# Kernel tuning notes

Hardware: AMD Instinct MI355X
Metric: run time of the kernel (lower is better)

Reference implementation:

```python
import jax, jax.numpy as jnp
import numpy as np

# Static problem structure (matches setup_inputs)
B, NPOLY, VPP, L = 32, 256, 64, 32
LAYERS = 3
PLEN = L * 2 ** LAYERS  # 256
LN_EPS = 1e-5


def _layernorm(h, g, b):
    mu = h.mean(-1, keepdims=True)
    var = ((h - mu) ** 2).mean(-1, keepdims=True)
    return g * (h - mu) / jnp.sqrt(var + LN_EPS) + b


def _forward(data, W0, b0, g0, beta0, W1, b1, g1, beta1, W2, b2, g2, beta2,
             Wq, bq, Wk, bk, Wv, bv):
    # row 0 holds agent polyline index in feature 0
    agent_id = data[:, 0, 0].astype(jnp.int32)  # [B]
    vecs = data[:, 1:, :]
    vecs = vecs.at[:, :, -1].set(0.0)  # zero out polyline-id feature (data[:,:,-1]=0)
    x = vecs.reshape(B, NPOLY, VPP, L)  # uniform polyline groups

    # SubGraph: 3 layers of (MLP -> maxpool aggregate -> concat), doubling width
    for (W, b, g, be) in ((W0, b0, g0, beta0), (W1, b1, g1, beta1), (W2, b2, g2, beta2)):
        h = jax.nn.relu(_layernorm(x @ W + b, g, be))  # [B,P,V,c]
        agg = h.max(axis=2, keepdims=True)             # [B,P,1,c]
        x = jnp.concatenate([h, jnp.broadcast_to(agg, h.shape)], axis=-1)  # [B,P,V,2c]
    P = x.max(axis=2)  # [B, NPOLY, PLEN] polyline features

    # Global graph: single-head attention with agent polyline as query
    q = P[jnp.arange(B), agent_id] @ Wq + bq          # [B, C]
    k = P @ Wk + bk                                    # [B, P, C]
    v = P @ Wv + bv
    scores = jnp.einsum('bc,bpc->bp', q, k) / jnp.sqrt(jnp.float32(PLEN))
    att = jax.nn.softmax(scores, axis=-1)
    return jnp.einsum('bp,bpc->bc', att, v)           # [B, PLEN]


def setup_inputs() -> dict:
    key = jax.random.key(0)
    ks = jax.random.split(key, 24)
    V = 1 + NPOLY * VPP
    data = jax.random.normal(ks[0], (B, V, L), dtype=jnp.float32)
    agent = jax.random.randint(ks[1], (B,), 0, NPOLY).astype(jnp.float32)
    data = data.at[:, 0, :].set(0.0).at[:, 0, 0].set(agent)
    pid = jnp.repeat(jnp.arange(NPOLY), VPP).astype(jnp.float32)
    data = data.at[:, 1:, -1].set(pid[None, :])

    inp = {'data': data}
    c = L
    for i in range(LAYERS):
        inp[f'W{i}'] = 0.02 * jax.random.normal(ks[2 + i], (c, c), dtype=jnp.float32)
        inp[f'b{i}'] = jnp.zeros((c,), jnp.float32)
        inp[f'g{i}'] = jnp.ones((c,), jnp.float32)
        inp[f'beta{i}'] = jnp.zeros((c,), jnp.float32)
        c *= 2
    C = PLEN
    for j, nm in enumerate(('q', 'k', 'v')):
        inp[f'W{nm}'] = 0.02 * jax.random.normal(ks[10 + j], (C, C), dtype=jnp.float32)
        inp[f'b{nm}'] = jnp.zeros((C,), jnp.float32)
    return inp


def reference(data, W0, b0, g0, beta0, W1, b1, g1, beta1, W2, b2, g2, beta2,
              Wq, bq, Wk, bk, Wv, bv):
    return _forward(data, W0, b0, g0, beta0, W1, b1, g1, beta1, W2, b2, g2, beta2,
                    Wq, bq, Wk, bk, Wv, bv)
```

## Files before the change

### kernel.cpp

```cpp
#include <hip/hip_runtime.h>

#define NPOLY 256
#define VPP   64
#define LCH   32
#define NV    (1 + NPOLY * VPP)
#define LN_EPS 1e-5f

typedef __bf16 bf16x8 __attribute__((ext_vector_type(8)));
typedef float  f32x4  __attribute__((ext_vector_type(4)));

union U4B8 { uint4 u; bf16x8 v; };

__device__ __forceinline__ unsigned packbf(float a, float b) {
    unsigned r;
    asm("v_cvt_pk_bf16_f32 %0, %1, %2" : "=v"(r) : "v"(a), "v"(b));
    return r;
}

__global__ void vn_prep1(const float* __restrict__ W0, const float* __restrict__ W1,
                         const float* __restrict__ W2,
                         const float* __restrict__ Wq, const float* __restrict__ Wk,
                         const float* __restrict__ Wv,
                         float* __restrict__ Wqf, float* __restrict__ Wkf,
                         float* __restrict__ Wvf, uint4* __restrict__ wpack)
{
    int t = blockIdx.x * 256 + threadIdx.x;
    if (t < 3 * 32768) {
        int which = t >> 15, r = t & 32767;
        const float* src = which == 0 ? Wq : which == 1 ? Wk : Wv;
        float*       dst = which == 0 ? Wqf : which == 1 ? Wkf : Wvf;
        dst[r] = src[r] + src[r + 128 * 256];
        return;
    }
    t -= 3 * 32768;
    if (t >= 22 * 64) return;
    int f = t >> 6, L = t & 63, q = L >> 4, m = L & 15;
    const float* src; int N, k0, col;
    if (f < 2)      { src = W0; N = 32;  k0 = q * 8;                 col = f * 16 + m; }
    else if (f < 6) { src = W1; N = 64;  k0 = q * 8;                 col = (f - 2) * 16 + m; }
    else { int g = f - 6; src = W2; N = 128; k0 = (g >> 3) * 32 + q * 8; col = (g & 7) * 16 + m; }
    float e[8];
    #pragma unroll
    for (int j = 0; j < 8; j++) e[j] = src[(k0 + j) * N + col];
    uint4 o;
    o.x = packbf(e[0], e[1]); o.y = packbf(e[2], e[3]);
    o.z = packbf(e[4], e[5]); o.w = packbf(e[6], e[7]);
    wpack[f * 64 + L] = o;
}

__global__ void vn_prep2(const float* __restrict__ Wqf, const float* __restrict__ Wkf,
                         const float* __restrict__ bq,
                         float* __restrict__ Mff, float* __restrict__ u0f)
{
    int t = blockIdx.x * 256 + threadIdx.x;
    if (t < 16384) {
        int i = t >> 7, j = t & 127;
        const float4* a = (const float4*)(Wqf + i * 256);
        const float4* b = (const float4*)(Wkf + j * 256);
        float s0 = 0.f, s1 = 0.f, s2 = 0.f, s3 = 0.f;
        #pragma unroll 4
        for (int c = 0; c < 64; c++) {
            float4 A = a[c], B = b[c];
            s0 = fmaf(A.x, B.x, s0); s1 = fmaf(A.y, B.y, s1);
            s2 = fmaf(A.z, B.z, s2); s3 = fmaf(A.w, B.w, s3);
        }
        Mff[i * 128 + j] = (s0 + s1) + (s2 + s3);
    } else if (t < 16512) {
        int j = t - 16384;
        const float4* a = (const float4*)bq;
        const float4* b = (const float4*)(Wkf + j * 256);
        float s0 = 0.f, s1 = 0.f, s2 = 0.f, s3 = 0.f;
        #pragma unroll 4
        for (int c = 0; c < 64; c++) {
            float4 A = a[c], B = b[c];
            s0 = fmaf(A.x, B.x, s0); s1 = fmaf(A.y, B.y, s1);
            s2 = fmaf(A.z, B.z, s2); s3 = fmaf(A.w, B.w, s3);
        }
        u0f[j] = (s0 + s1) + (s2 + s3);
    }
}

__global__ __launch_bounds__(64, 3) void vn_mlp(
    const float* __restrict__ data, const uint4* __restrict__ wpack,
    const float* __restrict__ b0, const float* __restrict__ g0, const float* __restrict__ be0,
    const float* __restrict__ W1, const float* __restrict__ b1,
    const float* __restrict__ g1, const float* __restrict__ be1,
    const float* __restrict__ W2, const float* __restrict__ b2,
    const float* __restrict__ g2, const float* __restrict__ be2,
    float* __restrict__ Ph)
{
    __shared__ __align__(16) unsigned short hbuf[64 * 72];
    __shared__ float fbuf[192];

    const int blk = blockIdx.x;
    const int L = threadIdx.x, q = L >> 4, m = L & 15;
    const int bb = blk >> 8, pp = blk & 255;

    const float* rowbase = data + ((size_t)bb * NV + 1 + (size_t)pp * VPP) * LCH;
    bf16x8 A0[4];
    #pragma unroll
    for (int rt = 0; rt < 4; rt++) {
        const float* rp = rowbase + (size_t)(rt * 16 + m) * LCH + q * 8;
        float4 u = *(const float4*)rp;
        float4 v = *(const float4*)(rp + 4);
        if (q == 3) v.w = 0.f;
        U4B8 c;
        c.u.x = packbf(u.x, u.y); c.u.y = packbf(u.z, u.w);
        c.u.z = packbf(v.x, v.y); c.u.w = packbf(v.z, v.w);
        A0[rt] = c.v;
    }
    U4B8 t0, t1; t0.u = wpack[0 * 64 + L]; t1.u = wpack[1 * 64 + L];
    float bc0[2] = { b0[m], b0[16 + m] };
    f32x4 acc0[4][2];
    #pragma unroll
    for (int rt = 0; rt < 4; rt++) {
        {
            f32x4 a = { bc0[0], bc0[0], bc0[0], bc0[0] };
            acc0[rt][0] = __builtin_amdgcn_mfma_f32_16x16x32_bf16(A0[rt], t0.v, a, 0, 0, 0);
        }
        {
            f32x4 a = { bc0[1], bc0[1], bc0[1], bc0[1] };
            acc0[rt][1] = __builtin_amdgcn_mfma_f32_16x16x32_bf16(A0[rt], t1.v, a, 0, 0, 0);
        }
    }
    float g0c[2]  = { g0[m],  g0[16 + m]  };
    float be0c[2] = { be0[m], be0[16 + m] };
    float a0mx[2] = { 0.f, 0.f };
    #pragma unroll
    for (int rt = 0; rt < 4; rt++) {
        #pragma unroll
        for (int reg = 0; reg < 4; reg++) {
            float x0 = acc0[rt][0][reg], x1 = acc0[rt][1][reg];
            float rs = x0 + x1, rq = x0 * x0 + x1 * x1;
            #pragma unroll
            for (int s = 1; s < 16; s <<= 1) { rs += __shfl_xor(rs, s, 64); rq += __shfl_xor(rq, s, 64); }
            float mu = rs * (1.f / 32.f);
            float var = rq * (1.f / 32.f) - mu * mu;
            float ri = rsqrtf(var + LN_EPS);
            #pragma unroll
            for (int ct = 0; ct < 2; ct++) {
                float v = fmaxf(fmaf(g0c[ct] * ri, acc0[rt][ct][reg] - mu, be0c[ct]), 0.f);
                acc0[rt][ct][reg] = v;
                a0mx[ct] = fmaxf(a0mx[ct], v);
            }
        }
    }
    #pragma unroll
    for (int ct = 0; ct < 2; ct++) {
        float v = a0mx[ct];
        v = fmaxf(v, __shfl_xor(v, 16, 64));
        v = fmaxf(v, __shfl_xor(v, 32, 64));
        a0mx[ct] = v;
    }
    if (q == 0) { fbuf[m] = a0mx[0]; fbuf[16 + m] = a0mx[1]; }
    __builtin_amdgcn_wave_barrier();
    float au1a = b1[L], au1b = 0.f;
    for (int j = 0; j < 32; j += 2) {
        au1a = fmaf(fbuf[j],     W1[(32 + j) * 64 + L],     au1a);
        au1b = fmaf(fbuf[j + 1], W1[(32 + j + 1) * 64 + L], au1b);
    }
    float au1 = au1a + au1b;
    #pragma unroll
    for (int rt = 0; rt < 4; rt++)
        #pragma unroll
        for (int reg = 0; reg < 4; reg++) {
            int row = rt * 16 + q * 4 + reg;
            unsigned u = packbf(acc0[rt][0][reg], acc0[rt][1][reg]);
            hbuf[row * 72 + m]      = (unsigned short)u;
            hbuf[row * 72 + 16 + m] = (unsigned short)(u >> 16);
        }
    __builtin_amdgcn_wave_barrier();
    fbuf[64 + L] = au1;
    __builtin_amdgcn_wave_barrier();

    bf16x8 A1[4];
    #pragma unroll
    for (int rt = 0; rt < 4; rt++) {
        U4B8 c; c.u = *(const uint4*)(hbuf + (rt * 16 + m) * 72 + q * 8);
        A1[rt] = c.v;
    }
    f32x4 acc1[4][4];
    #pragma unroll
    for (int ct = 0; ct < 4; ct++) {
        U4B8 wv; wv.u = wpack[(2 + ct) * 64 + L];
        float au = fbuf[64 + ct * 16 + m];
        #pragma unroll
        for (int rt = 0; rt < 4; rt++) {
            f32x4 a = { au, au, au, au };
            acc1[rt][ct] = __builtin_amdgcn_mfma_f32_16x16x32_bf16(A1[rt], wv.v, a, 0, 0, 0);
        }
    }
    float g1c[4], be1c[4];
    #pragma unroll
    for (int ct = 0; ct < 4; ct++) { g1c[ct] = g1[ct * 16 + m]; be1c[ct] = be1[ct * 16 + m]; }
    float a1mx[4] = { 0.f, 0.f, 0.f, 0.f };
    #pragma unroll
    for (int rt = 0; rt < 4; rt++) {
        #pragma unroll
        for (int reg = 0; reg < 4; reg++) {
            float rs = 0.f, rq = 0.f;
            #pragma unroll
            for (int ct = 0; ct < 4; ct++) { float x = acc1[rt][ct][reg]; rs += x; rq += x * x; }
            #pragma unroll
            for (int s = 1; s < 16; s <<= 1) { rs += __shfl_xor(rs, s, 64); rq += __shfl_xor(rq, s, 64); }
            float mu = rs * (1.f / 64.f);
            float var = rq * (1.f / 64.f) - mu * mu;
            float ri = rsqrtf(var + LN_EPS);
            #pragma unroll
            for (int ct = 0; ct < 4; ct++) {
                float v = fmaxf(fmaf(g1c[ct] * ri, acc1[rt][ct][reg] - mu, be1c[ct]), 0.f);
                acc1[rt][ct][reg] = v;
                a1mx[ct] = fmaxf(a1mx[ct], v);
            }
        }
    }
    #pragma unroll
    for (int ct = 0; ct < 4; ct++) {
        float v = a1mx[ct];
        v = fmaxf(v, __shfl_xor(v, 16, 64));
        v = fmaxf(v, __shfl_xor(v, 32, 64));
        a1mx[ct] = v;
    }
    __builtin_amdgcn_wave_barrier();
    if (q == 0) {
        #pragma unroll
        for (int ct = 0; ct < 4; ct++) fbuf[ct * 16 + m] = a1mx[ct];
    }
    __builtin_amdgcn_wave_barrier();
    float au2a = b2[L], au2b = b2[64 + L], au2c = 0.f, au2d = 0.f;
    for (int j = 0; j < 64; j += 2) {
        float av0 = fbuf[j], av1 = fbuf[j + 1];
        au2a = fmaf(av0, W2[(64 + j) * 128 + L],          au2a);
        au2b = fmaf(av0, W2[(64 + j) * 128 + 64 + L],     au2b);
        au2c = fmaf(av1, W2[(64 + j + 1) * 128 + L],      au2c);
        au2d = fmaf(av1, W2[(64 + j + 1) * 128 + 64 + L], au2d);
    }
    au2a += au2c; au2b += au2d;
    #pragma unroll
    for (int rt = 0; rt < 4; rt++)
        #pragma unroll
        for (int reg = 0; reg < 4; reg++) {
            int row = rt * 16 + q * 4 + reg;
            unsigned ua = packbf(acc1[rt][0][reg], acc1[rt][1][reg]);
            unsigned ub = packbf(acc1[rt][2][reg], acc1[rt][3][reg]);
            hbuf[row * 72 + m]      = (unsigned short)ua;
            hbuf[row * 72 + 16 + m] = (unsigned short)(ua >> 16);
            hbuf[row * 72 + 32 + m] = (unsigned short)ub;
            hbuf[row * 72 + 48 + m] = (unsigned short)(ub >> 16);
        }
    __builtin_amdgcn_wave_barrier();
    fbuf[64 + L] = au2a; fbuf[128 + L] = au2b;
    __builtin_amdgcn_wave_barrier();

    bf16x8 A2[4][2];
    #pragma unroll
    for (int rt = 0; rt < 4; rt++)
        #pragma unroll
        for (int ks = 0; ks < 2; ks++) {
            U4B8 c; c.u = *(const uint4*)(hbuf + (rt * 16 + m) * 72 + ks * 32 + q * 8);
            A2[rt][ks] = c.v;
        }
    f32x4 rsum[4] = {}, rqsum[4] = {};
    #pragma unroll
    for (int ct = 0; ct < 8; ct++) {
        U4B8 wa, wb;
        wa.u = wpack[(6 + ct) * 64 + L];
        wb.u = wpack[(14 + ct) * 64 + L];
        float au = fbuf[64 + ct * 16 + m];
        #pragma unroll
        for (int rt = 0; rt < 4; rt++) {
            f32x4 a = { au, au, au, au };
            a = __builtin_amdgcn_mfma_f32_16x16x32_bf16(A2[rt][0], wa.v, a, 0, 0, 0);
            a = __builtin_amdgcn_mfma_f32_16x16x32_bf16(A2[rt][1], wb.v, a, 0, 0, 0);
            rsum[rt] += a;
            rqsum[rt] += a * a;
        }
    }
    f32x4 muv[4], riv[4];
    #pragma unroll
    for (int rt = 0; rt < 4; rt++) {
        #pragma unroll
        for (int reg = 0; reg < 4; reg++) {
            float rs = rsum[rt][reg], rq = rqsum[rt][reg];
            #pragma unroll
            for (int s = 1; s < 16; s <<= 1) { rs += __shfl_xor(rs, s, 64); rq += __shfl_xor(rq, s, 64); }
            float mu = rs * (1.f / 128.f);
            float var = rq * (1.f / 128.f) - mu * mu;
            muv[rt][reg] = mu;
            riv[rt][reg] = rsqrtf(var + LN_EPS);
        }
    }
    float g2c[8], be2c[8];
    #pragma unroll
    for (int ct = 0; ct < 8; ct++) { g2c[ct] = g2[ct * 16 + m]; be2c[ct] = be2[ct * 16 + m]; }
    float m2[8] = { 0.f, 0.f, 0.f, 0.f, 0.f, 0.f, 0.f, 0.f };
    #pragma unroll
    for (int ct = 0; ct < 8; ct++) {
        U4B8 wa, wb;
        wa.u = wpack[(6 + ct) * 64 + L];
        wb.u = wpack[(14 + ct) * 64 + L];
        float au = fbuf[64 + ct * 16 + m];
        #pragma unroll
        for (int rt = 0; rt < 4; rt++) {
            f32x4 a = { au, au, au, au };
            a = __builtin_amdgcn_mfma_f32_16x16x32_bf16(A2[rt][0], wa.v, a, 0, 0, 0);
            a = __builtin_amdgcn_mfma_f32_16x16x32_bf16(A2[rt][1], wb.v, a, 0, 0, 0);
            #pragma unroll
            for (int reg = 0; reg < 4; reg++) {
                float v = fmaxf(fmaf(g2c[ct] * riv[rt][reg], a[reg] - muv[rt][reg], be2c[ct]), 0.f);
                m2[ct] = fmaxf(m2[ct], v);
            }
        }
    }
    #pragma unroll
    for (int ct = 0; ct < 8; ct++) {
        float v = m2[ct];
        v = fmaxf(v, __shfl_xor(v, 16, 64));
        v = fmaxf(v, __shfl_xor(v, 32, 64));
        m2[ct] = v;
    }
    float v1 = q == 0 ? m2[0] : q == 1 ? m2[1] : q == 2 ? m2[2] : m2[3];
    float v2 = q == 0 ? m2[4] : q == 1 ? m2[5] : q == 2 ? m2[6] : m2[7];
    float* op = Ph + (size_t)blk * 128;
    op[L] = v1; op[64 + L] = v2;
}

__global__ __launch_bounds__(256) void vn_attn(
    const float* __restrict__ data, const float* __restrict__ Ph,
    const float* __restrict__ Mff, const float* __restrict__ u0f,
    const float* __restrict__ Wvf, const float* __restrict__ bv,
    float* __restrict__ out)
{
    __shared__ __align__(16) float pah[128], tts[128], att[256], pb[128];
    __shared__ __align__(16) float part[256];
    __shared__ float red[8];
    const int b = blockIdx.x, tid = threadIdx.x, lane = tid & 63, wave = tid >> 6;
    const float* PhB = Ph + (size_t)b * NPOLY * 128;
    const int agent = (int)data[(size_t)b * NV * LCH];

    if (tid < 128) pah[tid] = PhB[(size_t)agent * 128 + tid];
    __syncthreads();

    {
        const int j = tid & 127, h = tid >> 7;
        const float* mc = Mff + (size_t)(h * 64) * 128 + j;
        const float* pv = pah + h * 64;
        float s0 = 0.f, s1 = 0.f, s2 = 0.f, s3 = 0.f;
        for (int i = 0; i < 64; i += 4) {
            s0 = fmaf(pv[i],     mc[(i)     * 128], s0);
            s1 = fmaf(pv[i + 1], mc[(i + 1) * 128], s1);
            s2 = fmaf(pv[i + 2], mc[(i + 2) * 128], s2);
            s3 = fmaf(pv[i + 3], mc[(i + 3) * 128], s3);
        }
        part[tid] = (s0 + s1) + (s2 + s3);
    }
    __syncthreads();
    if (tid < 128) tts[tid] = part[tid] + part[128 + tid] + u0f[tid];
    __syncthreads();

    float sv;
    {
        const float* pr = PhB + (size_t)tid * 128;
        float s0 = 0.f, s1 = 0.f, s2 = 0.f, s3 = 0.f;
        for (int j = 0; j < 128; j += 16) {
            float4 x0 = *(const float4*)(pr + j);
            float4 x1 = *(const float4*)(pr + j + 4);
            float4 x2 = *(const float4*)(pr + j + 8);
            float4 x3 = *(const float4*)(pr + j + 12);
            float4 t0 = *(const float4*)(tts + j);
            float4 t1 = *(const float4*)(tts + j + 4);
            float4 t2 = *(const float4*)(tts + j + 8);
            float4 t3 = *(const float4*)(tts + j + 12);
            s0 = fmaf(x0.w, t0.w, fmaf(x0.z, t0.z, fmaf(x0.y, t0.y, fmaf(x0.x, t0.x, s0))));
            s1 = fmaf(x1.w, t1.w, fmaf(x1.z, t1.z, fmaf(x1.y, t1.y, fmaf(x1.x, t1.x, s1))));
            s2 = fmaf(x2.w, t2.w, fmaf(x2.z, t2.z, fmaf(x2.y, t2.y, fmaf(x2.x, t2.x, s2))));
            s3 = fmaf(x3.w, t3.w, fmaf(x3.z, t3.z, fmaf(x3.y, t3.y, fmaf(x3.x, t3.x, s3))));
        }
        sv = ((s0 + s1) + (s2 + s3)) * 0.0625f;
    }
    float mx = sv;
    #pragma unroll
    for (int s = 1; s < 64; s <<= 1) mx = fmaxf(mx, __shfl_xor(mx, s, 64));
    if (lane == 0) red[wave] = mx;
    __syncthreads();
    mx = fmaxf(fmaxf(red[0], red[1]), fmaxf(red[2], red[3]));
    float e = expf(sv - mx);
    float sm = e;
    #pragma unroll
    for (int s = 1; s < 64; s <<= 1) sm += __shfl_xor(sm, s, 64);
    if (lane == 0) red[4 + wave] = sm;
    __syncthreads();
    const float tot = red[4] + red[5] + red[6] + red[7];
    att[tid] = e / tot;
    __syncthreads();

    {
        const int c = tid & 127, h = tid >> 7;
        const float* pp = PhB + (size_t)(h * 128) * 128 + c;
        const float* ap = att + h * 128;
        float s0 = 0.f, s1 = 0.f, s2 = 0.f, s3 = 0.f;
        for (int p = 0; p < 128; p += 4) {
            s0 = fmaf(ap[p],     pp[(p)     * 128], s0);
            s1 = fmaf(ap[p + 1], pp[(p + 1) * 128], s1);
            s2 = fmaf(ap[p + 2], pp[(p + 2) * 128], s2);
            s3 = fmaf(ap[p + 3], pp[(p + 3) * 128], s3);
        }
        part[tid] = (s0 + s1) + (s2 + s3);
    }
    __syncthreads();
    if (tid < 128) pb[tid] = part[tid] + part[128 + tid];
    __syncthreads();

    {
        const float* wv = Wvf + tid;
        float s0 = 0.f, s1 = 0.f, s2 = 0.f, s3 = 0.f;
        for (int j = 0; j < 128; j += 4) {
            s0 = fmaf(pb[j],     wv[(j)     * 256], s0);
            s1 = fmaf(pb[j + 1], wv[(j + 1) * 256], s1);
            s2 = fmaf(pb[j + 2], wv[(j + 2) * 256], s2);
            s3 = fmaf(pb[j + 3], wv[(j + 3) * 256], s3);
        }
        out[(size_t)b * 256 + tid] = bv[tid] + ((s0 + s1) + (s2 + s3));
    }
}

extern "C" void kernel_launch(void* const* d_in, const int* in_sizes, int n_in,
                              void* d_out, int out_size, void* d_ws, size_t ws_size,
                              hipStream_t stream)
{
    const float* data = (const float*)d_in[0];
    const float* W0 = (const float*)d_in[1];
    const float* b0 = (const float*)d_in[2];
    const float* g0 = (const float*)d_in[3];
    const float* be0= (const float*)d_in[4];
    const float* W1 = (const float*)d_in[5];
    const float* b1 = (const float*)d_in[6];
    const float* g1 = (const float*)d_in[7];
    const float* be1= (const float*)d_in[8];
    const float* W2 = (const float*)d_in[9];
    const float* b2 = (const float*)d_in[10];
    const float* g2 = (const float*)d_in[11];
    const float* be2= (const float*)d_in[12];
    const float* Wq = (const float*)d_in[13];
    const float* bq = (const float*)d_in[14];
    const float* Wk = (const float*)d_in[15];
    const float* bk = (const float*)d_in[16];
    const float* Wv = (const float*)d_in[17];
    const float* bv = (const float*)d_in[18];
    (void)bk;

    char* wsb = (char*)d_ws;
    float* Ph    = (float*)(wsb);
    float* Wqf   = (float*)(wsb + 4194304);
    float* Wkf   = (float*)(wsb + 4325376);
    float* Wvf   = (float*)(wsb + 4456448);
    float* Mff   = (float*)(wsb + 4587520);
    float* u0f   = (float*)(wsb + 4653056);
    uint4* wpack = (uint4*)(wsb + 4653568);

    vn_prep1<<<390, 256, 0, stream>>>(W0, W1, W2, Wq, Wk, Wv, Wqf, Wkf, Wvf, wpack);
    vn_prep2<<<65, 256, 0, stream>>>(Wqf, Wkf, bq, Mff, u0f);
    vn_mlp<<<32 * NPOLY, 64, 0, stream>>>(data, wpack,
                                          b0, g0, be0,
                                          W1, b1, g1, be1,
                                          W2, b2, g2, be2, Ph);
    vn_attn<<<32, 256, 0, stream>>>(data, Ph, Mff, u0f, Wvf, bv, (float*)d_out);
}
```

Baseline: 234.1 us.

## Split per-polyline MLP across four waves with shared-memory max and matvec reductions

Each polyline block moves from a single 64-thread wave that handled all four 16-row tiles to four waves of 256 threads, one row tile each. The cross-row max-pool and the aggregate matvec through W1 and W2 are now split across the waves through shared partial buffers and block-level barriers. Because each wave now holds all layer-2 accumulators in registers, the second MFMA pass used for layernorm in layer 2 is dropped. The aim is more parallelism and fewer registers per wave, at the price of several __syncthreads per block and more shared memory.

Result: faster. 209.8 us (-10.4%).

```diff
diff --git a/kernel.cpp b/kernel.cpp
--- a/kernel.cpp
+++ b/kernel.cpp
@@ -80,7 +80,7 @@
     }
 }
 
-__global__ __launch_bounds__(64, 3) void vn_mlp(
+__global__ __launch_bounds__(256, 3) void vn_mlp(
     const float* __restrict__ data, const uint4* __restrict__ wpack,
     const float* __restrict__ b0, const float* __restrict__ g0, const float* __restrict__ be0,
     const float* __restrict__ W1, const float* __restrict__ b1,
@@ -90,47 +90,43 @@
     float* __restrict__ Ph)
 {
     __shared__ __align__(16) unsigned short hbuf[64 * 72];
-    __shared__ float fbuf[192];
-
+    __shared__ float partA[4][128];
+    __shared__ float partB[4][128];
+
+    const int tid = threadIdx.x;
+    const int w = tid >> 6, L = tid & 63, q = L >> 4, m = L & 15;
     const int blk = blockIdx.x;
-    const int L = threadIdx.x, q = L >> 4, m = L & 15;
     const int bb = blk >> 8, pp = blk & 255;
+    const int r0 = w * 16;
 
     const float* rowbase = data + ((size_t)bb * NV + 1 + (size_t)pp * VPP) * LCH;
-    bf16x8 A0[4];
-    #pragma unroll
-    for (int rt = 0; rt < 4; rt++) {
-        const float* rp = rowbase + (size_t)(rt * 16 + m) * LCH + q * 8;
+    bf16x8 A0;
+    {
+        const float* rp = rowbase + (size_t)(r0 + m) * LCH + q * 8;
         float4 u = *(const float4*)rp;
         float4 v = *(const float4*)(rp + 4);
         if (q == 3) v.w = 0.f;
         U4B8 c;
         c.u.x = packbf(u.x, u.y); c.u.y = packbf(u.z, u.w);
         c.u.z = packbf(v.x, v.y); c.u.w = packbf(v.z, v.w);
-        A0[rt] = c.v;
-    }
-    U4B8 t0, t1; t0.u = wpack[0 * 64 + L]; t1.u = wpack[1 * 64 + L];
-    float bc0[2] = { b0[m], b0[16 + m] };
-    f32x4 acc0[4][2];
-    #pragma unroll
-    for (int rt = 0; rt < 4; rt++) {
-        {
-            f32x4 a = { bc0[0], bc0[0], bc0[0], bc0[0] };
-            acc0[rt][0] = __builtin_amdgcn_mfma_f32_16x16x32_bf16(A0[rt], t0.v, a, 0, 0, 0);
-        }
-        {
-            f32x4 a = { bc0[1], bc0[1], bc0[1], bc0[1] };
-            acc0[rt][1] = __builtin_amdgcn_mfma_f32_16x16x32_bf16(A0[rt], t1.v, a, 0, 0, 0);
-        }
-    }
-    float g0c[2]  = { g0[m],  g0[16 + m]  };
-    float be0c[2] = { be0[m], be0[16 + m] };
-    float a0mx[2] = { 0.f, 0.f };
-    #pragma unroll
-    for (int rt = 0; rt < 4; rt++) {
+        A0 = c.v;
+    }
+    f32x4 acc0[2];
+    {
+        U4B8 t0, t1; t0.u = wpack[0 * 64 + L]; t1.u = wpack[1 * 64 + L];
+        float bca = b0[m], bcb = b0[16 + m];
+        f32x4 a0 = { bca, bca, bca, bca };
+        f32x4 a1 = { bcb, bcb, bcb, bcb };
+        acc0[0] = __builtin_amdgcn_mfma_f32_16x16x32_bf16(A0, t0.v, a0, 0, 0, 0);
+        acc0[1] = __builtin_amdgcn_mfma_f32_16x16x32_bf16(A0, t1.v, a1, 0, 0, 0);
+    }
+    {
+        float g0c[2]  = { g0[m],  g0[16 + m]  };
+        float be0c[2] = { be0[m], be0[16 + m] };
+        float a0mx[2] = { 0.f, 0.f };
         #pragma unroll
         for (int reg = 0; reg < 4; reg++) {
-            float x0 = acc0[rt][0][reg], x1 = acc0[rt][1][reg];
+            float x0 = acc0[0][reg], x1 = acc0[1][reg];
             float rs = x0 + x1, rq = x0 * x0 + x1 * x1;
             #pragma unroll
             for (int s = 1; s < 16; s <<= 1) { rs += __shfl_xor(rs, s, 64); rq += __shfl_xor(rq, s, 64); }
@@ -139,68 +135,63 @@
             float ri = rsqrtf(var + LN_EPS);
             #pragma unroll
             for (int ct = 0; ct < 2; ct++) {
-                float v = fmaxf(fmaf(g0c[ct] * ri, acc0[rt][ct][reg] - mu, be0c[ct]), 0.f);
-                acc0[rt][ct][reg] = v;
+                float v = fmaxf(fmaf(g0c[ct] * ri, acc0[ct][reg] - mu, be0c[ct]), 0.f);
+                acc0[ct][reg] = v;
                 a0mx[ct] = fmaxf(a0mx[ct], v);
             }
         }
-    }
-    #pragma unroll
-    for (int ct = 0; ct < 2; ct++) {
-        float v = a0mx[ct];
-        v = fmaxf(v, __shfl_xor(v, 16, 64));
-        v = fmaxf(v, __shfl_xor(v, 32, 64));
-        a0mx[ct] = v;
-    }
-    if (q == 0) { fbuf[m] = a0mx[0]; fbuf[16 + m] = a0mx[1]; }
-    __builtin_amdgcn_wave_barrier();
-    float au1a = b1[L], au1b = 0.f;
-    for (int j = 0; j < 32; j += 2) {
-        au1a = fmaf(fbuf[j],     W1[(32 + j) * 64 + L],     au1a);
-        au1b = fmaf(fbuf[j + 1], W1[(32 + j + 1) * 64 + L], au1b);
-    }
-    float au1 = au1a + au1b;
-    #pragma unroll
-    for (int rt = 0; rt < 4; rt++)
-        #pragma unroll
-        for (int reg = 0; reg < 4; reg++) {
-            int row = rt * 16 + q * 4 + reg;
-            unsigned u = packbf(acc0[rt][0][reg], acc0[rt][1][reg]);
-            hbuf[row * 72 + m]      = (unsigned short)u;
-            hbuf[row * 72 + 16 + m] = (unsigned short)(u >> 16);
-        }
-    __builtin_amdgcn_wave_barrier();
-    fbuf[64 + L] = au1;
-    __builtin_amdgcn_wave_barrier();
-
-    bf16x8 A1[4];
-    #pragma unroll
-    for (int rt = 0; rt < 4; rt++) {
-        U4B8 c; c.u = *(const uint4*)(hbuf + (rt * 16 + m) * 72 + q * 8);
-        A1[rt] = c.v;
-    }
-    f32x4 acc1[4][4];
+        #pragma unroll
+        for (int ct = 0; ct < 2; ct++) {
+            float v = a0mx[ct];
+            v = fmaxf(v, __shfl_xor(v, 16, 64));
+            v = fmaxf(v, __shfl_xor(v, 32, 64));
+            a0mx[ct] = v;
+        }
+        if (q == 0) { partA[w][m] = a0mx[0]; partA[w][16 + m] = a0mx[1]; }
+    }
+    #pragma unroll
+    for (int reg = 0; reg < 4; reg++) {
+        int row = r0 + q * 4 + reg;
+        unsigned u = packbf(acc0[0][reg], acc0[1][reg]);
+        hbuf[row * 72 + m]      = (unsigned short)u;
+        hbuf[row * 72 + 16 + m] = (unsigned short)(u >> 16);
+    }
+    __syncthreads();
+
+    {
+        float p = 0.f;
+        int j0 = w * 8;
+        #pragma unroll
+        for (int jj = 0; jj < 8; jj++) {
+            int j = j0 + jj;
+            float a = fmaxf(fmaxf(partA[0][j], partA[1][j]), fmaxf(partA[2][j], partA[3][j]));
+            p = fmaf(a, W1[(32 + j) * 64 + L], p);
+        }
+        partB[w][L] = p;
+    }
+    __syncthreads();
+
+    bf16x8 A1;
+    { U4B8 c; c.u = *(const uint4*)(hbuf + (r0 + m) * 72 + q * 8); A1 = c.v; }
+    f32x4 acc1[4];
     #pragma unroll
     for (int ct = 0; ct < 4; ct++) {
         U4B8 wv; wv.u = wpack[(2 + ct) * 64 + L];
-        float au = fbuf[64 + ct * 16 + m];
-        #pragma unroll
-        for (int rt = 0; rt < 4; rt++) {
-            f32x4 a = { au, au, au, au };
-            acc1[rt][ct] = __builtin_amdgcn_mfma_f32_16x16x32_bf16(A1[rt], wv.v, a, 0, 0, 0);
-        }
-    }
-    float g1c[4], be1c[4];
-    #pragma unroll
-    for (int ct = 0; ct < 4; ct++) { g1c[ct] = g1[ct * 16 + m]; be1c[ct] = be1[ct * 16 + m]; }
-    float a1mx[4] = { 0.f, 0.f, 0.f, 0.f };
-    #pragma unroll
-    for (int rt = 0; rt < 4; rt++) {
+        int n = ct * 16 + m;
+        float au = b1[n] + ((partB[0][n] + partB[1][n]) + (partB[2][n] + partB[3][n]));
+        f32x4 a = { au, au, au, au };
+        acc1[ct] = __builtin_amdgcn_mfma_f32_16x16x32_bf16(A1, wv.v, a, 0, 0, 0);
+    }
+    {
+        float g1c[4], be1c[4];
+        #pragma unroll
+        for (int ct = 0; ct < 4; ct++) { g1c[ct] = g1[ct * 16 + m]; be1c[ct] = be1[ct * 16 + m]; }
+        float a1mx[4] = { 0.f, 0.f, 0.f, 0.f };
         #pragma unroll
         for (int reg = 0; reg < 4; reg++) {
             float rs = 0.f, rq = 0.f;
             #pragma unroll
-            for (int ct = 0; ct < 4; ct++) { float x = acc1[rt][ct][reg]; rs += x; rq += x * x; }
+            for (int ct = 0; ct < 4; ct++) { float x = acc1[ct][reg]; rs += x; rq += x * x; }
             #pragma unroll
             for (int s = 1; s < 16; s <<= 1) { rs += __shfl_xor(rs, s, 64); rq += __shfl_xor(rq, s, 64); }
             float mu = rs * (1.f / 64.f);
@@ -208,121 +199,109 @@
             float ri = rsqrtf(var + LN_EPS);
             #pragma unroll
             for (int ct = 0; ct < 4; ct++) {
-                float v = fmaxf(fmaf(g1c[ct] * ri, acc1[rt][ct][reg] - mu, be1c[ct]), 0.f);
-                acc1[rt][ct][reg] = v;
+                float v = fmaxf(fmaf(g1c[ct] * ri, acc1[ct][reg] - mu, be1c[ct]), 0.f);
+                acc1[ct][reg] = v;
                 a1mx[ct] = fmaxf(a1mx[ct], v);
             }
         }
-    }
-    #pragma unroll
-    for (int ct = 0; ct < 4; ct++) {
-        float v = a1mx[ct];
-        v = fmaxf(v, __shfl_xor(v, 16, 64));
-        v = fmaxf(v, __shfl_xor(v, 32, 64));
-        a1mx[ct] = v;
-    }
-    __builtin_amdgcn_wave_barrier();
-    if (q == 0) {
-        #pragma unroll
-        for (int ct = 0; ct < 4; ct++) fbuf[ct * 16 + m] = a1mx[ct];
-    }
-    __builtin_amdgcn_wave_barrier();
-    float au2a = b2[L], au2b = b2[64 + L], au2c = 0.f, au2d = 0.f;
-    for (int j = 0; j < 64; j += 2) {
-        float av0 = fbuf[j], av1 = fbuf[j + 1];
-        au2a = fmaf(av0, W2[(64 + j) * 128 + L],          au2a);
-        au2b = fmaf(av0, W2[(64 + j) * 128 + 64 + L],     au2b);
-        au2c = fmaf(av1, W2[(64 + j + 1) * 128 + L],      au2c);
-        au2d = fmaf(av1, W2[(64 + j + 1) * 128 + 64 + L], au2d);
-    }
-    au2a += au2c; au2b += au2d;
-    #pragma unroll
-    for (int rt = 0; rt < 4; rt++)
-        #pragma unroll
-        for (int reg = 0; reg < 4; reg++) {
-            int row = rt * 16 + q * 4 + reg;
-            unsigned ua = packbf(acc1[rt][0][reg], acc1[rt][1][reg]);
-            unsigned ub = packbf(acc1[rt][2][reg], acc1[rt][3][reg]);
-            hbuf[row * 72 + m]      = (unsigned short)ua;
-            hbuf[row * 72 + 16 + m] = (unsigned short)(ua >> 16);
-            hbuf[row * 72 + 32 + m] = (unsigned short)ub;
-            hbuf[row * 72 + 48 + m] = (unsigned short)(ub >> 16);
-        }
-    __builtin_amdgcn_wave_barrier();
-    fbuf[64 + L] = au2a; fbuf[128 + L] = au2b;
-    __builtin_amdgcn_wave_barrier();
-
-    bf16x8 A2[4][2];
-    #pragma unroll
-    for (int rt = 0; rt < 4; rt++)
-        #pragma unroll
-        for (int ks = 0; ks < 2; ks++) {
-            U4B8 c; c.u = *(const uint4*)(hbuf + (rt * 16 + m) * 72 + ks * 32 + q * 8);
-            A2[rt][ks] = c.v;
-        }
-    f32x4 rsum[4] = {}, rqsum[4] = {};
+        #pragma unroll
+        for (int ct = 0; ct < 4; ct++) {
+            float v = a1mx[ct];
+            v = fmaxf(v, __shfl_xor(v, 16, 64));
+            v = fmaxf(v, __shfl_xor(v, 32, 64));
+            a1mx[ct] = v;
+        }
+        if (q == 0) {
+            #pragma unroll
+            for (int ct = 0; ct < 4; ct++) partA[w][ct * 16 + m] = a1mx[ct];
+        }
+    }
+    #pragma unroll
+    for (int reg = 0; reg < 4; reg++) {
+        int row = r0 + q * 4 + reg;
+        unsigned ua = packbf(acc1[0][reg], acc1[1][reg]);
+        unsigned ub = packbf(acc1[2][reg], acc1[3][reg]);
+        hbuf[row * 72 + m]      = (unsigned short)ua;
+        hbuf[row * 72 + 16 + m] = (unsigned short)(ua >> 16);
+        hbuf[row * 72 + 32 + m] = (unsigned short)ub;
+        hbuf[row * 72 + 48 + m] = (unsigned short)(ub >> 16);
+    }
+    __syncthreads();
+
+    {
+        float pa = 0.f, pb = 0.f;
+        int j0 = w * 16;
+        #pragma unroll
+        for (int jj = 0; jj < 16; jj++) {
+            int j = j0 + jj;
+            float a = fmaxf(fmaxf(partA[0][j], partA[1][j]), fmaxf(partA[2][j], partA[3][j]));
+            pa = fmaf(a, W2[(64 + j) * 128 + L],      pa);
+            pb = fmaf(a, W2[(64 + j) * 128 + 64 + L], pb);
+        }
+        partB[w][L]      = pa;
+        partB[w][64 + L] = pb;
+    }
+    __syncthreads();
+
+    bf16x8 A2[2];
+    #pragma unroll
+    for (int ks = 0; ks < 2; ks++) {
+        U4B8 c; c.u = *(const uint4*)(hbuf + (r0 + m) * 72 + ks * 32 + q * 8);
+        A2[ks] = c.v;
+    }
+    f32x4 acc2[8];
     #pragma unroll
     for (int ct = 0; ct < 8; ct++) {
         U4B8 wa, wb;
         wa.u = wpack[(6 + ct) * 64 + L];
         wb.u = wpack[(14 + ct) * 64 + L];
-        float au = fbuf[64 + ct * 16 + m];
-        #pragma unroll
-        for (int rt = 0; rt < 4; rt++) {
-            f32x4 a = { au, au, au, au };
-            a = __builtin_amdgcn_mfma_f32_16x16x32_bf16(A2[rt][0], wa.v, a, 0, 0, 0);
-            a = __builtin_amdgcn_mfma_f32_16x16x32_bf16(A2[rt][1], wb.v, a, 0, 0, 0);
-            rsum[rt] += a;
-            rqsum[rt] += a * a;
-        }
-    }
-    f32x4 muv[4], riv[4];
-    #pragma unroll
-    for (int rt = 0; rt < 4; rt++) {
+        int n = ct * 16 + m;
+        float au = b2[n] + ((partB[0][n] + partB[1][n]) + (partB[2][n] + partB[3][n]));
+        f32x4 a = { au, au, au, au };
+        a = __builtin_amdgcn_mfma_f32_16x16x32_bf16(A2[0], wa.v, a, 0, 0, 0);
+        a = __builtin_amdgcn_mfma_f32_16x16x32_bf16(A2[1], wb.v, a, 0, 0, 0);
+        acc2[ct] = a;
+    }
+    {
+        float g2c[8], be2c[8];
+        #pragma unroll
+        for (int ct = 0; ct < 8; ct++) { g2c[ct] = g2[ct * 16 + m]; be2c[ct] = be2[ct * 16 + m]; }
+        float m2[8] = { 0.f, 0.f, 0.f, 0.f, 0.f, 0.f, 0.f, 0.f };
         #pragma unroll
         for (int reg = 0; reg < 4; reg++) {
-            float rs = rsum[rt][reg], rq = rqsum[rt][reg];
+            float rs = 0.f, rq = 0.f;
+            #pragma unroll
+            for (int ct = 0; ct < 8; ct++) { float x = acc2[ct][reg]; rs += x; rq += x * x; }
             #pragma unroll
             for (int s = 1; s < 16; s <<= 1) { rs += __shfl_xor(rs, s, 64); rq += __shfl_xor(rq, s, 64); }
             float mu = rs * (1.f / 128.f);
             float var = rq * (1.f / 128.f) - mu * mu;
-            muv[rt][reg] = mu;
-            riv[rt][reg] = rsqrtf(var + LN_EPS);
-        }
-    }
-    float g2c[8], be2c[8];
-    #pragma unroll
-    for (int ct = 0; ct < 8; ct++) { g2c[ct] = g2[ct * 16 + m]; be2c[ct] = be2[ct * 16 + m]; }
-    float m2[8] = { 0.f, 0.f, 0.f, 0.f, 0.f, 0.f, 0.f, 0.f };
-    #pragma unroll
-    for (int ct = 0; ct < 8; ct++) {
-        U4B8 wa, wb;
-        wa.u = wpack[(6 + ct) * 64 + L];
-        wb.u = wpack[(14 + ct) * 64 + L];
-        float au = fbuf[64 + ct * 16 + m];
-        #pragma unroll
-        for (int rt = 0; rt < 4; rt++) {
-            f32x4 a = { au, au, au, au };
-            a = __builtin_amdgcn_mfma_f32_16x16x32_bf16(A2[rt][0], wa.v, a, 0, 0, 0);
-            a = __builtin_amdgcn_mfma_f32_16x16x32_bf16(A2[rt][1], wb.v, a, 0, 0, 0);
-            #pragma unroll
-            for (int reg = 0; reg < 4; reg++) {
-                float v = fmaxf(fmaf(g2c[ct] * riv[rt][reg], a[reg] - muv[rt][reg], be2c[ct]), 0.f);
+            float ri = rsqrtf(var + LN_EPS);
+            #pragma unroll
+            for (int ct = 0; ct < 8; ct++) {
+                float v = fmaxf(fmaf(g2c[ct] * ri, acc2[ct][reg] - mu, be2c[ct]), 0.f);
                 m2[ct] = fmaxf(m2[ct], v);
             }
         }
-    }
-    #pragma unroll
-    for (int ct = 0; ct < 8; ct++) {
-        float v = m2[ct];
-        v = fmaxf(v, __shfl_xor(v, 16, 64));
-        v = fmaxf(v, __shfl_xor(v, 32, 64));
-        m2[ct] = v;
-    }
-    float v1 = q == 0 ? m2[0] : q == 1 ? m2[1] : q == 2 ? m2[2] : m2[3];
-    float v2 = q == 0 ? m2[4] : q == 1 ? m2[5] : q == 2 ? m2[6] : m2[7];
-    float* op = Ph + (size_t)blk * 128;
-    op[L] = v1; op[64 + L] = v2;
+        #pragma unroll
+        for (int ct = 0; ct < 8; ct++) {
+            float v = m2[ct];
+            v = fmaxf(v, __shfl_xor(v, 16, 64));
+            v = fmaxf(v, __shfl_xor(v, 32, 64));
+            m2[ct] = v;
+        }
+        if (q == 0) {
+            #pragma unroll
+            for (int ct = 0; ct < 8; ct++) partA[w][ct * 16 + m] = m2[ct];
+        }
+    }
+    __syncthreads();
+
+    if (tid < 128) {
+        float v = fmaxf(fmaxf(partA[0][tid], partA[1][tid]),
+                        fmaxf(partA[2][tid], partA[3][tid]));
+        Ph[(size_t)blk * 128 + tid] = v;
+    }
 }
 
 __global__ __launch_bounds__(256) void vn_attn(
@@ -460,9 +439,9 @@
 
     vn_prep1<<<390, 256, 0, stream>>>(W0, W1, W2, Wq, Wk, Wv, Wqf, Wkf, Wvf, wpack);
     vn_prep2<<<65, 256, 0, stream>>>(Wqf, Wkf, bq, Mff, u0f);
-    vn_mlp<<<32 * NPOLY, 64, 0, stream>>>(data, wpack,
-                                          b0, g0, be0,
-                                          W1, b1, g1, be1,
-                                          W2, b2, g2, be2, Ph);
+    vn_mlp<<<32 * NPOLY, 256, 0, stream>>>(data, wpack,
+                                           b0, g0, be0,
+                                           W1, b1, g1, be1,
+                                           W2, b2, g2, be2, Ph);
     vn_attn<<<32, 256, 0, stream>>>(data, Ph, Mff, u0f, Wvf, bv, (float*)d_out);
 }
```
